# Kernel tuning notes

Measured on AMD Instinct MI355X. Metric: run time of the kernel, lower is better.

## Reference

```python
import jax, jax.numpy as jnp
import numpy as np


def setup_inputs() -> dict:
    key = jax.random.key(0)
    k1, k2 = jax.random.split(key)
    x = jax.random.normal(k1, (16384, 2048), dtype=jnp.float32)
    diag_elements = jax.random.normal(k2, (2048,), dtype=jnp.float32)
    return {"x": x, "diag_elements": diag_elements}


def reference(x, diag_elements):
    # Original: jnp.dot(x, jnp.diag(diag_elements)).
    # Mathematically identical to scaling each column of x by the
    # corresponding diagonal element (broadcast multiply).
    return x * diag_elements
```

## Files before the change

### kernel.cpp

```cpp
#include <hip/hip_runtime.h>

__global__ __launch_bounds__(256) void DiagonalDense_kernel(
    const float4* __restrict__ x,
    const float4* __restrict__ diag,
    float4* __restrict__ out,
    int n4) {
    int i = blockIdx.x * blockDim.x + threadIdx.x;
    if (i < n4) {
        float4 xv = x[i];
        float4 dv = diag[i & 511];
        float4 ov;
        ov.x = xv.x * dv.x;
        ov.y = xv.y * dv.y;
        ov.z = xv.z * dv.z;
        ov.w = xv.w * dv.w;
        out[i] = ov;
    }
}

extern "C" void kernel_launch(void* const* d_in, const int* in_sizes, int n_in,
                              void* d_out, int out_size, void* d_ws, size_t ws_size,
                              hipStream_t stream) {
    const float4* x    = (const float4*)d_in[0];
    const float4* diag = (const float4*)d_in[1];
    float4* out        = (float4*)d_out;

    const int n  = out_size;
    const int n4 = n / 4;
    const int block = 256;
    const int grid  = (n4 + block - 1) / block;

    DiagonalDense_kernel<<<grid, block, 0, stream>>>(x, diag, out, n4);
}
```

Baseline: 221.5 us.

## Use grid-stride loop with hoisted diag load and nontemporal stores

```diff
diff --git a/kernel.cpp b/kernel.cpp
--- a/kernel.cpp
+++ b/kernel.cpp
@@ -1,34 +1,36 @@
 #include <hip/hip_runtime.h>
 
+using f4 = __attribute__((ext_vector_type(4))) float;
+
 __global__ __launch_bounds__(256) void DiagonalDense_kernel(
-    const float4* __restrict__ x,
-    const float4* __restrict__ diag,
-    float4* __restrict__ out,
+    const f4* __restrict__ x,
+    const f4* __restrict__ diag,
+    f4* __restrict__ out,
     int n4) {
-    int i = blockIdx.x * blockDim.x + threadIdx.x;
-    if (i < n4) {
-        float4 xv = x[i];
-        float4 dv = diag[i & 511];
-        float4 ov;
-        ov.x = xv.x * dv.x;
-        ov.y = xv.y * dv.y;
-        ov.z = xv.z * dv.z;
-        ov.w = xv.w * dv.w;
-        out[i] = ov;
+    const int i0     = blockIdx.x * blockDim.x + threadIdx.x;
+    const int stride = gridDim.x * blockDim.x;
+
+    const f4 dv = diag[i0 & 511];
+
+    #pragma unroll 4
+    for (int i = i0; i < n4; i += stride) {
+        f4 xv = x[i];
+        f4 ov = xv * dv;
+        __builtin_nontemporal_store(ov, &out[i]);
     }
 }
 
 extern "C" void kernel_launch(void* const* d_in, const int* in_sizes, int n_in,
                               void* d_out, int out_size, void* d_ws, size_t ws_size,
                               hipStream_t stream) {
-    const float4* x    = (const float4*)d_in[0];
-    const float4* diag = (const float4*)d_in[1];
-    float4* out        = (float4*)d_out;
+    const f4* x    = (const f4*)d_in[0];
+    const f4* diag = (const f4*)d_in[1];
+    f4* out        = (f4*)d_out;
 
     const int n  = out_size;
     const int n4 = n / 4;
+
     const int block = 256;
-    const int grid  = (n4 + block - 1) / block;
-
+    const int grid  = 2048;
     DiagonalDense_kernel<<<grid, block, 0, stream>>>(x, diag, out, n4);
 }
```

Result: slower. 238.2 us (+7.5%).
